# Kernel tuning notes

Hardware: AMD Instinct MI355X
Metric: run time of the kernel (lower is better)

Reference implementation:

```python
import jax, jax.numpy as jnp
import numpy as np

N, D, K = 65536, 512, 4096


def setup_inputs() -> dict:
    key = jax.random.key(0)
    kx, kc = jax.random.split(key)
    x = jax.random.normal(kx, (N, D), dtype=jnp.float32)
    center = jax.random.normal(kc, (K, D), dtype=jnp.float32)
    return {"x": x, "center": center}


def squared_euclidean(x, center):
    x_sq = jnp.sum(x * x, axis=1, keepdims=True)        # [N,1]
    c_sq = jnp.sum(center * center, axis=1)             # [K]
    cross = x @ center.T                                # [N,K] GEMM
    return x_sq - 2.0 * cross + c_sq[None, :]


def reference(x, center):
    # KMeans.forward: dis_func(input, center).argmin(1)
    dist = squared_euclidean(x, center)                 # [N,K]
    return jnp.argmin(dist, axis=1)                     # [N] int32
```

## Files before the change

### kernel.cpp

```cpp
#include <hip/hip_runtime.h>

#define N_ROWS 65536
#define DIM    512
#define K_CENT 4096
#define TILE_M 128
#define TILE_N 128
#define BK     32
#define KSTEPS (DIM / BK)
#define NKT    (K_CENT / TILE_N)
#define THREADS 512
#define MARGIN 6.0f
#define CAND_CAP 3072
#define COMPACT_TRIG 2048

typedef _Float16 half8 __attribute__((ext_vector_type(8)));
typedef float floatx4 __attribute__((ext_vector_type(4)));

__device__ __forceinline__ unsigned mapF(float f) {
  unsigned u = __float_as_uint(f);
  return (u & 0x80000000u) ? ~u : (u | 0x80000000u);
}
__device__ __forceinline__ float unmapF(unsigned m) {
  unsigned u = (m & 0x80000000u) ? (m ^ 0x80000000u) : ~m;
  return __uint_as_float(u);
}

__device__ __forceinline__ void gload_lds16(const void* g, void* l) {
  __builtin_amdgcn_global_load_lds(
      (const __attribute__((address_space(1))) void*)g,
      (__attribute__((address_space(3))) void*)l, 16, 0, 0);
}

__global__ void prep_convert(const float* __restrict__ x, const float* __restrict__ c,
                             _Float16* __restrict__ xh, _Float16* __restrict__ ch) {
  const size_t nx = (size_t)N_ROWS * DIM;
  const size_t nc = (size_t)K_CENT * DIM;
  size_t i = ((size_t)blockIdx.x * blockDim.x + threadIdx.x) * 8;
  if (i >= nx + nc) return;
  const float* src;
  _Float16* dst;
  if (i < nx) { src = x + i; dst = xh + i; }
  else        { src = c + (i - nx); dst = ch + (i - nx); }
  floatx4 a = *(const floatx4*)src;
  floatx4 b = *(const floatx4*)(src + 4);
  half8 h;
#pragma unroll
  for (int e = 0; e < 4; ++e) { h[e] = (_Float16)a[e]; h[4 + e] = (_Float16)b[e]; }
  *(half8*)dst = h;
}

__global__ void prep_csq(const _Float16* __restrict__ ch, float* __restrict__ csqg) {
  int w = (int)((blockIdx.x * blockDim.x + threadIdx.x) >> 6);
  int lane = threadIdx.x & 63;
  if (w >= K_CENT) return;
  half8 h = *(const half8*)(ch + (size_t)w * DIM + lane * 8);
  float s = 0.f;
#pragma unroll
  for (int e = 0; e < 8; ++e) { float v = (float)h[e]; s += v * v; }
#pragma unroll
  for (int off = 1; off < 64; off <<= 1) s += __shfl_xor(s, off, 64);
  if (lane == 0) csqg[w] = s;
}

template <int MODE>
__global__ __launch_bounds__(THREADS, 4)
void kmeans_argmin(const float* __restrict__ x, const float* __restrict__ cent,
                   const _Float16* __restrict__ xh, const _Float16* __restrict__ ch,
                   const float* __restrict__ csqg, int* __restrict__ out) {
  __shared__ _Float16 ldsA[TILE_M * BK];
  __shared__ _Float16 ldsB[TILE_N * BK];
  __shared__ float csq4[TILE_N][4];
  __shared__ unsigned sminU[TILE_M];
  __shared__ unsigned long long best[TILE_M];
  __shared__ unsigned candKey[CAND_CAP];
  __shared__ float candS[CAND_CAP];
  __shared__ int candCount;

  char* ldsAc = (char*)ldsA;
  char* ldsBc = (char*)ldsB;

  const int t = threadIdx.x;
  const int lane = t & 63;
  const int wave = t >> 6;
  const int wm = wave >> 1;
  const int wn = wave & 1;
  const int quad = lane >> 4;
  const int l15 = lane & 15;
  const int rowBlock = blockIdx.x * TILE_M;

  if (t < TILE_M) { sminU[t] = 0xFFFFFFFFu; best[t] = ~0ull; }
  if (t == 0) candCount = 0;

  const int sr = t >> 2;
  const int sck = (t & 3) ^ ((sr >> 1) & 3);

  float thrR[2][4];

  for (int kt = 0; kt < NKT; ++kt) {
    const int ktBase = kt * TILE_N;
    if (MODE <= 1) csq4[t >> 2][t & 3] = 0.f;
    floatx4 acc[2][4];
#pragma unroll
    for (int fm = 0; fm < 2; ++fm)
#pragma unroll
      for (int fn = 0; fn < 4; ++fn) acc[fm][fn] = (floatx4){0.f, 0.f, 0.f, 0.f};

    for (int ks = 0; ks < KSTEPS; ++ks) {
      const int kd = ks * BK;
      if (MODE >= 1) {
        gload_lds16(xh + (size_t)(rowBlock + sr) * DIM + kd + sck * 8,
                    ldsAc + (size_t)wave * 1024);
        gload_lds16(ch + (size_t)(ktBase + sr) * DIM + kd + sck * 8,
                    ldsBc + (size_t)wave * 1024);
        __syncthreads();
        if (MODE == 1) {
          half8 hb = *(const half8*)(ldsBc + (size_t)t * 16);
          float s = 0.f;
#pragma unroll
          for (int e = 0; e < 8; ++e) { float v = (float)hb[e]; s += v * v; }
          csq4[sr][t & 3] += s;
        }
      } else {
        const float* gA = x + (size_t)(rowBlock + sr) * DIM + kd + sck * 8;
        const float* gB = cent + (size_t)(ktBase + sr) * DIM + kd + sck * 8;
        floatx4 a0 = *(const floatx4*)gA, a1 = *(const floatx4*)(gA + 4);
        floatx4 b0 = *(const floatx4*)gB, b1 = *(const floatx4*)(gB + 4);
        half8 ha, hb;
        float s = 0.f;
#pragma unroll
        for (int e = 0; e < 4; ++e) {
          ha[e] = (_Float16)a0[e]; ha[4 + e] = (_Float16)a1[e];
          hb[e] = (_Float16)b0[e]; hb[4 + e] = (_Float16)b1[e];
        }
#pragma unroll
        for (int e = 0; e < 8; ++e) { float v = (float)hb[e]; s += v * v; }
        *(half8*)(ldsAc + (size_t)t * 16) = ha;
        *(half8*)(ldsBc + (size_t)t * 16) = hb;
        csq4[sr][t & 3] += s;
        __syncthreads();
      }

      half8 af[2], bf[4];
#pragma unroll
      for (int fm = 0; fm < 2; ++fm) {
        int row = wm * 32 + fm * 16 + l15;
        int slot = (row << 2) | (quad ^ ((row >> 1) & 3));
        af[fm] = *(const half8*)(ldsAc + slot * 16);
      }
#pragma unroll
      for (int fn = 0; fn < 4; ++fn) {
        int cl = wn * 64 + fn * 16 + l15;
        int slot = (cl << 2) | (quad ^ ((cl >> 1) & 3));
        bf[fn] = *(const half8*)(ldsBc + slot * 16);
      }
#pragma unroll
      for (int fm = 0; fm < 2; ++fm)
#pragma unroll
        for (int fn = 0; fn < 4; ++fn)
          acc[fm][fn] = __builtin_amdgcn_mfma_f32_16x16x32_f16(af[fm], bf[fn], acc[fm][fn], 0, 0, 0);
      __syncthreads();
    }

    float cs[4];
#pragma unroll
    for (int fn = 0; fn < 4; ++fn) {
      int cl = wn * 64 + fn * 16 + l15;
      cs[fn] = (MODE == 2) ? csqg[ktBase + cl]
                           : (csq4[cl][0] + csq4[cl][1] + csq4[cl][2] + csq4[cl][3]);
    }
    float tmin[2][4];
#pragma unroll
    for (int fm = 0; fm < 2; ++fm)
#pragma unroll
      for (int e = 0; e < 4; ++e) tmin[fm][e] = 3.4e38f;
#pragma unroll
    for (int fn = 0; fn < 4; ++fn)
#pragma unroll
      for (int fm = 0; fm < 2; ++fm)
#pragma unroll
        for (int e = 0; e < 4; ++e) {
          float s = cs[fn] - 2.f * acc[fm][fn][e];
          tmin[fm][e] = fminf(tmin[fm][e], s);
        }

    if (kt == 0) {
#pragma unroll
      for (int fm = 0; fm < 2; ++fm)
#pragma unroll
        for (int e = 0; e < 4; ++e)
          atomicMin(&sminU[wm * 32 + fm * 16 + quad * 4 + e], mapF(tmin[fm][e]));
      __syncthreads();
    }
#pragma unroll
    for (int fm = 0; fm < 2; ++fm)
#pragma unroll
      for (int e = 0; e < 4; ++e)
        thrR[fm][e] = unmapF(sminU[wm * 32 + fm * 16 + quad * 4 + e]) + MARGIN;

#pragma unroll
    for (int fn = 0; fn < 4; ++fn) {
      int k = ktBase + wn * 64 + fn * 16 + l15;
#pragma unroll
      for (int fm = 0; fm < 2; ++fm)
#pragma unroll
        for (int e = 0; e < 4; ++e) {
          float s = cs[fn] - 2.f * acc[fm][fn][e];
          if (s <= thrR[fm][e]) {
            int idx = atomicAdd(&candCount, 1);
            if (idx < CAND_CAP) {
              candKey[idx] = ((unsigned)k << 7) | (unsigned)(wm * 32 + fm * 16 + quad * 4 + e);
              candS[idx] = s;
            }
          }
        }
    }
    if (kt != 0) {
#pragma unroll
      for (int fm = 0; fm < 2; ++fm)
#pragma unroll
        for (int e = 0; e < 4; ++e)
          atomicMin(&sminU[wm * 32 + fm * 16 + quad * 4 + e], mapF(tmin[fm][e]));
    }
    __syncthreads();

    if (candCount > COMPACT_TRIG) {
      int cc = candCount; if (cc > CAND_CAP) cc = CAND_CAP;
      unsigned myK[6]; float myS[6]; int myN = 0;
      for (int i = t; i < cc; i += THREADS) {
        int rl = candKey[i] & 127;
        if (candS[i] <= unmapF(sminU[rl]) + MARGIN) {
          myK[myN] = candKey[i]; myS[myN] = candS[i]; ++myN;
        }
      }
      __syncthreads();
      if (t == 0) candCount = 0;
      __syncthreads();
      int base = atomicAdd(&candCount, myN);
      for (int j = 0; j < myN; ++j) { candKey[base + j] = myK[j]; candS[base + j] = myS[j]; }
      __syncthreads();
    }
  }

  int cnt = candCount; if (cnt > CAND_CAP) cnt = CAND_CAP;
  const int g = t >> 4;
  const int sl = t & 15;
  for (int ci = g; ci < cnt; ci += 32) {
    unsigned cd = candKey[ci];
    int rl = cd & 127;
    if (candS[ci] > unmapF(sminU[rl]) + MARGIN) continue;
    int k = cd >> 7;
    const float* xr = x + (size_t)(rowBlock + rl) * DIM;
    const float* cr = cent + (size_t)k * DIM;
    double d = 0.0;
#pragma unroll
    for (int j = 0; j < DIM / 64; ++j) {
      floatx4 xv = *(const floatx4*)(xr + j * 64 + sl * 4);
      floatx4 cv = *(const floatx4*)(cr + j * 64 + sl * 4);
#pragma unroll
      for (int e = 0; e < 4; ++e) {
        double df = (double)xv[e] - (double)cv[e];
        d += df * df;
      }
    }
#pragma unroll
    for (int off = 1; off < 16; off <<= 1) d += __shfl_xor(d, off, 64);
    if (sl == 0) {
      unsigned long long key =
          ((unsigned long long)__double_as_longlong(d) & ~0xFFFull) | (unsigned long long)k;
      atomicMin(&best[rl], key);
    }
  }
  __syncthreads();
  if (t < TILE_M) out[rowBlock + t] = (int)(best[t] & 0xFFFull);
}

extern "C" void kernel_launch(void* const* d_in, const int* in_sizes, int n_in,
                              void* d_out, int out_size, void* d_ws, size_t ws_size,
                              hipStream_t stream) {
  const float* x = (const float*)d_in[0];
  const float* cent = (const float*)d_in[1];
  int* out = (int*)d_out;
  const size_t nXh = (size_t)N_ROWS * DIM * sizeof(_Float16);
  const size_t nCh = (size_t)K_CENT * DIM * sizeof(_Float16);
  const size_t nCsq = (size_t)K_CENT * sizeof(float);
  const int grid = N_ROWS / TILE_M;

  if (ws_size >= nXh + nCh + nCsq) {
    _Float16* xh = (_Float16*)d_ws;
    _Float16* ch = (_Float16*)((char*)d_ws + nXh);
    float* csqg = (float*)((char*)d_ws + nXh + nCh);
    const size_t total8 = ((size_t)N_ROWS + K_CENT) * DIM / 8;
    prep_convert<<<(unsigned)((total8 + 255) / 256), 256, 0, stream>>>(x, cent, xh, ch);
    prep_csq<<<(K_CENT * 64) / 256, 256, 0, stream>>>(ch, csqg);
    kmeans_argmin<2><<<grid, THREADS, 0, stream>>>(x, cent, xh, ch, csqg, out);
  } else if (ws_size >= nXh + nCh) {
    _Float16* xh = (_Float16*)d_ws;
    _Float16* ch = (_Float16*)((char*)d_ws + nXh);
    const size_t total8 = ((size_t)N_ROWS + K_CENT) * DIM / 8;
    prep_convert<<<(unsigned)((total8 + 255) / 256), 256, 0, stream>>>(x, cent, xh, ch);
    kmeans_argmin<1><<<grid, THREADS, 0, stream>>>(x, cent, xh, ch, nullptr, out);
  } else {
    kmeans_argmin<0><<<grid, THREADS, 0, stream>>>(x, cent, nullptr, nullptr, nullptr, out);
  }
}
```

Measured before the change: 740.7 us.

## Widen centroid tile to 256, fuse csq into convert, reduce min via shuffles

```diff
diff --git a/kernel.cpp b/kernel.cpp
--- a/kernel.cpp
+++ b/kernel.cpp
@@ -4,7 +4,7 @@
 #define DIM    512
 #define K_CENT 4096
 #define TILE_M 128
-#define TILE_N 128
+#define TILE_N 256
 #define BK     32
 #define KSTEPS (DIM / BK)
 #define NKT    (K_CENT / TILE_N)
@@ -32,34 +32,34 @@
 }
 
 __global__ void prep_convert(const float* __restrict__ x, const float* __restrict__ c,
-                             _Float16* __restrict__ xh, _Float16* __restrict__ ch) {
+                             _Float16* __restrict__ xh, _Float16* __restrict__ ch,
+                             float* __restrict__ csqg) {
   const size_t nx = (size_t)N_ROWS * DIM;
   const size_t nc = (size_t)K_CENT * DIM;
   size_t i = ((size_t)blockIdx.x * blockDim.x + threadIdx.x) * 8;
   if (i >= nx + nc) return;
-  const float* src;
-  _Float16* dst;
-  if (i < nx) { src = x + i; dst = xh + i; }
-  else        { src = c + (i - nx); dst = ch + (i - nx); }
-  floatx4 a = *(const floatx4*)src;
-  floatx4 b = *(const floatx4*)(src + 4);
-  half8 h;
-#pragma unroll
-  for (int e = 0; e < 4; ++e) { h[e] = (_Float16)a[e]; h[4 + e] = (_Float16)b[e]; }
-  *(half8*)dst = h;
-}
-
-__global__ void prep_csq(const _Float16* __restrict__ ch, float* __restrict__ csqg) {
-  int w = (int)((blockIdx.x * blockDim.x + threadIdx.x) >> 6);
-  int lane = threadIdx.x & 63;
-  if (w >= K_CENT) return;
-  half8 h = *(const half8*)(ch + (size_t)w * DIM + lane * 8);
-  float s = 0.f;
-#pragma unroll
-  for (int e = 0; e < 8; ++e) { float v = (float)h[e]; s += v * v; }
-#pragma unroll
-  for (int off = 1; off < 64; off <<= 1) s += __shfl_xor(s, off, 64);
-  if (lane == 0) csqg[w] = s;
+  if (i < nx) {
+    floatx4 a = *(const floatx4*)(x + i);
+    floatx4 b = *(const floatx4*)(x + i + 4);
+    half8 h;
+#pragma unroll
+    for (int e = 0; e < 4; ++e) { h[e] = (_Float16)a[e]; h[4 + e] = (_Float16)b[e]; }
+    *(half8*)(xh + i) = h;
+  } else {
+    size_t off = i - nx;
+    floatx4 a = *(const floatx4*)(c + off);
+    floatx4 b = *(const floatx4*)(c + off + 4);
+    half8 h;
+    float s = 0.f;
+#pragma unroll
+    for (int e = 0; e < 4; ++e) { h[e] = (_Float16)a[e]; h[4 + e] = (_Float16)b[e]; }
+#pragma unroll
+    for (int e = 0; e < 8; ++e) { float v = (float)h[e]; s += v * v; }
+    *(half8*)(ch + off) = h;
+#pragma unroll
+    for (int o = 1; o < 64; o <<= 1) s += __shfl_xor(s, o, 64);
+    if ((threadIdx.x & 63) == 0) csqg[off >> 9] = s;
+  }
 }
 
 template <int MODE>
@@ -82,8 +82,8 @@
   const int t = threadIdx.x;
   const int lane = t & 63;
   const int wave = t >> 6;
-  const int wm = wave >> 1;
-  const int wn = wave & 1;
+  const int wm = wave >> 2;
+  const int wn = wave & 3;
   const int quad = lane >> 4;
   const int l15 = lane & 15;
   const int rowBlock = blockIdx.x * TILE_M;
@@ -91,59 +91,61 @@
   if (t < TILE_M) { sminU[t] = 0xFFFFFFFFu; best[t] = ~0ull; }
   if (t == 0) candCount = 0;
 
-  const int sr = t >> 2;
-  const int sck = (t & 3) ^ ((sr >> 1) & 3);
-
-  float thrR[2][4];
+  const int srA = t >> 2;
+  const int sckA = (t & 3) ^ ((srA >> 1) & 3);
+  const int srB0 = t >> 2;
+  const int srB1 = (t + 512) >> 2;
+  const int sckB0 = (t & 3) ^ ((srB0 >> 1) & 3);
+  const int sckB1 = (t & 3) ^ ((srB1 >> 1) & 3);
 
   for (int kt = 0; kt < NKT; ++kt) {
     const int ktBase = kt * TILE_N;
-    if (MODE <= 1) csq4[t >> 2][t & 3] = 0.f;
-    floatx4 acc[2][4];
-#pragma unroll
-    for (int fm = 0; fm < 2; ++fm)
+    if (MODE == 0) { ((float*)csq4)[t] = 0.f; ((float*)csq4)[t + 512] = 0.f; }
+    floatx4 acc[4][4];
+#pragma unroll
+    for (int fm = 0; fm < 4; ++fm)
 #pragma unroll
       for (int fn = 0; fn < 4; ++fn) acc[fm][fn] = (floatx4){0.f, 0.f, 0.f, 0.f};
 
     for (int ks = 0; ks < KSTEPS; ++ks) {
       const int kd = ks * BK;
-      if (MODE >= 1) {
-        gload_lds16(xh + (size_t)(rowBlock + sr) * DIM + kd + sck * 8,
+      if (MODE == 2) {
+        gload_lds16(xh + (size_t)(rowBlock + srA) * DIM + kd + sckA * 8,
                     ldsAc + (size_t)wave * 1024);
-        gload_lds16(ch + (size_t)(ktBase + sr) * DIM + kd + sck * 8,
+        gload_lds16(ch + (size_t)(ktBase + srB0) * DIM + kd + sckB0 * 8,
                     ldsBc + (size_t)wave * 1024);
-        __syncthreads();
-        if (MODE == 1) {
-          half8 hb = *(const half8*)(ldsBc + (size_t)t * 16);
+        gload_lds16(ch + (size_t)(ktBase + srB1) * DIM + kd + sckB1 * 8,
+                    ldsBc + 8192 + (size_t)wave * 1024);
+      } else {
+        const float* gA = x + (size_t)(rowBlock + srA) * DIM + kd + sckA * 8;
+        floatx4 a0 = *(const floatx4*)gA, a1 = *(const floatx4*)(gA + 4);
+        half8 ha;
+#pragma unroll
+        for (int e = 0; e < 4; ++e) { ha[e] = (_Float16)a0[e]; ha[4 + e] = (_Float16)a1[e]; }
+        *(half8*)(ldsAc + (size_t)t * 16) = ha;
+#pragma unroll
+        for (int p = 0; p < 2; ++p) {
+          int sr = p ? srB1 : srB0;
+          int sck = p ? sckB1 : sckB0;
+          int slot = p * 512 + t;
+          const float* gB = cent + (size_t)(ktBase + sr) * DIM + kd + sck * 8;
+          floatx4 b0 = *(const floatx4*)gB, b1 = *(const floatx4*)(gB + 4);
+          half8 hb;
           float s = 0.f;
 #pragma unroll
+          for (int e = 0; e < 4; ++e) { hb[e] = (_Float16)b0[e]; hb[4 + e] = (_Float16)b1[e]; }
+#pragma unroll
           for (int e = 0; e < 8; ++e) { float v = (float)hb[e]; s += v * v; }
-          csq4[sr][t & 3] += s;
+          *(half8*)(ldsBc + (size_t)slot * 16) = hb;
+          csq4[sr][slot & 3] += s;
         }
-      } else {
-        const float* gA = x + (size_t)(rowBlock + sr) * DIM + kd + sck * 8;
-        const float* gB = cent + (size_t)(ktBase + sr) * DIM + kd + sck * 8;
-        floatx4 a0 = *(const floatx4*)gA, a1 = *(const floatx4*)(gA + 4);
-        floatx4 b0 = *(const floatx4*)gB, b1 = *(const floatx4*)(gB + 4);
-        half8 ha, hb;
-        float s = 0.f;
-#pragma unroll
-        for (int e = 0; e < 4; ++e) {
-          ha[e] = (_Float16)a0[e]; ha[4 + e] = (_Float16)a1[e];
-          hb[e] = (_Float16)b0[e]; hb[4 + e] = (_Float16)b1[e];
-        }
-#pragma unroll
-        for (int e = 0; e < 8; ++e) { float v = (float)hb[e]; s += v * v; }
-        *(half8*)(ldsAc + (size_t)t * 16) = ha;
-        *(half8*)(ldsBc + (size_t)t * 16) = hb;
-        csq4[sr][t & 3] += s;
-        __syncthreads();
-      }
-
-      half8 af[2], bf[4];
-#pragma unroll
-      for (int fm = 0; fm < 2; ++fm) {
-        int row = wm * 32 + fm * 16 + l15;
+      }
+      __syncthreads();
+
+      half8 af[4], bf[4];
+#pragma unroll
+      for (int fm = 0; fm < 4; ++fm) {
+        int row = wm * 64 + fm * 16 + l15;
         int slot = (row << 2) | (quad ^ ((row >> 1) & 3));
         af[fm] = *(const half8*)(ldsAc + slot * 16);
       }
@@ -154,7 +156,7 @@
         bf[fn] = *(const half8*)(ldsBc + slot * 16);
       }
 #pragma unroll
-      for (int fm = 0; fm < 2; ++fm)
+      for (int fm = 0; fm < 4; ++fm)
 #pragma unroll
         for (int fn = 0; fn < 4; ++fn)
           acc[fm][fn] = __builtin_amdgcn_mfma_f32_16x16x32_f16(af[fm], bf[fn], acc[fm][fn], 0, 0, 0);
@@ -168,58 +170,47 @@
       cs[fn] = (MODE == 2) ? csqg[ktBase + cl]
                            : (csq4[cl][0] + csq4[cl][1] + csq4[cl][2] + csq4[cl][3]);
     }
-    float tmin[2][4];
-#pragma unroll
-    for (int fm = 0; fm < 2; ++fm)
-#pragma unroll
-      for (int e = 0; e < 4; ++e) tmin[fm][e] = 3.4e38f;
-#pragma unroll
-    for (int fn = 0; fn < 4; ++fn)
-#pragma unroll
-      for (int fm = 0; fm < 2; ++fm)
-#pragma unroll
-        for (int e = 0; e < 4; ++e) {
-          float s = cs[fn] - 2.f * acc[fm][fn][e];
-          tmin[fm][e] = fminf(tmin[fm][e], s);
-        }
-
-    if (kt == 0) {
-#pragma unroll
-      for (int fm = 0; fm < 2; ++fm)
-#pragma unroll
-        for (int e = 0; e < 4; ++e)
-          atomicMin(&sminU[wm * 32 + fm * 16 + quad * 4 + e], mapF(tmin[fm][e]));
-      __syncthreads();
-    }
-#pragma unroll
-    for (int fm = 0; fm < 2; ++fm)
+
+#pragma unroll
+    for (int fm = 0; fm < 4; ++fm)
+#pragma unroll
+      for (int e = 0; e < 4; ++e) {
+        float v = 3.4e38f;
+#pragma unroll
+        for (int fn = 0; fn < 4; ++fn)
+          v = fminf(v, cs[fn] - 2.f * acc[fm][fn][e]);
+        v = fminf(v, __shfl_xor(v, 1, 64));
+        v = fminf(v, __shfl_xor(v, 2, 64));
+        v = fminf(v, __shfl_xor(v, 4, 64));
+        v = fminf(v, __shfl_xor(v, 8, 64));
+        if (l15 == 0)
+          atomicMin(&sminU[wm * 64 + fm * 16 + quad * 4 + e], mapF(v));
+      }
+    __syncthreads();
+
+    float thrR[4][4];
+#pragma unroll
+    for (int fm = 0; fm < 4; ++fm)
 #pragma unroll
       for (int e = 0; e < 4; ++e)
-        thrR[fm][e] = unmapF(sminU[wm * 32 + fm * 16 + quad * 4 + e]) + MARGIN;
+        thrR[fm][e] = unmapF(sminU[wm * 64 + fm * 16 + quad * 4 + e]) + MARGIN;
 
 #pragma unroll
     for (int fn = 0; fn < 4; ++fn) {
       int k = ktBase + wn * 64 + fn * 16 + l15;
 #pragma unroll
-      for (int fm = 0; fm < 2; ++fm)
+      for (int fm = 0; fm < 4; ++fm)
 #pragma unroll
         for (int e = 0; e < 4; ++e) {
           float s = cs[fn] - 2.f * acc[fm][fn][e];
           if (s <= thrR[fm][e]) {
             int idx = atomicAdd(&candCount, 1);
             if (idx < CAND_CAP) {
-              candKey[idx] = ((unsigned)k << 7) | (unsigned)(wm * 32 + fm * 16 + quad * 4 + e);
+              candKey[idx] = ((unsigned)k << 7) | (unsigned)(wm * 64 + fm * 16 + quad * 4 + e);
               candS[idx] = s;
             }
           }
         }
-    }
-    if (kt != 0) {
-#pragma unroll
-      for (int fm = 0; fm < 2; ++fm)
-#pragma unroll
-        for (int e = 0; e < 4; ++e)
-          atomicMin(&sminU[wm * 32 + fm * 16 + quad * 4 + e], mapF(tmin[fm][e]));
     }
     __syncthreads();
 
@@ -290,15 +281,8 @@
     _Float16* ch = (_Float16*)((char*)d_ws + nXh);
     float* csqg = (float*)((char*)d_ws + nXh + nCh);
     const size_t total8 = ((size_t)N_ROWS + K_CENT) * DIM / 8;
-    prep_convert<<<(unsigned)((total8 + 255) / 256), 256, 0, stream>>>(x, cent, xh, ch);
-    prep_csq<<<(K_CENT * 64) / 256, 256, 0, stream>>>(ch, csqg);
+    prep_convert<<<(unsigned)((total8 + 255) / 256), 256, 0, stream>>>(x, cent, xh, ch, csqg);
     kmeans_argmin<2><<<grid, THREADS, 0, stream>>>(x, cent, xh, ch, csqg, out);
-  } else if (ws_size >= nXh + nCh) {
-    _Float16* xh = (_Float16*)d_ws;
-    _Float16* ch = (_Float16*)((char*)d_ws + nXh);
-    const size_t total8 = ((size_t)N_ROWS + K_CENT) * DIM / 8;
-    prep_convert<<<(unsigned)((total8 + 255) / 256), 256, 0, stream>>>(x, cent, xh, ch);
-    kmeans_argmin<1><<<grid, THREADS, 0, stream>>>(x, cent, xh, ch, nullptr, out);
   } else {
     kmeans_argmin<0><<<grid, THREADS, 0, stream>>>(x, cent, nullptr, nullptr, nullptr, out);
   }
```

After: 683.0 us. 1.08x faster.
